# Kernel optimization log

Hardware: AMD Instinct MI355X
Metric: run time of the kernel (lower is better)

Reference implementation:

```python
import jax, jax.numpy as jnp
import numpy as np

KERNEL_LEN = 512
INPUT_LEN = 65536


def setup_inputs() -> dict:
    key = jax.random.key(0)
    k1, k2 = jax.random.split(key)
    x = jax.random.normal(k1, (INPUT_LEN,), dtype=jnp.float32)
    kernel = jax.random.normal(k2, (KERNEL_LEN,), dtype=jnp.float32)
    return {"input": x, "kernel": kernel}


def _dtw_row(prev, d_row):
    # prev: accumulated_cost of previous row, shape [K]
    # ac[j] = min(prev[j-1], prev[j], ac[j-1]) + d[j]
    # Let c[j] = min(prev[j-1], prev[j]) + d[j]  (prev[-1] treated as +inf,
    # which reproduces ac[i,0] = prev[0] + d[0]).
    # Then ac[j] = min(c[j], ac[j-1] + d[j])
    #            = S[j] + cummin_k<=j (c[k] - S[k]),  S = inclusive cumsum of d.
    inf = jnp.full((1,), jnp.inf, dtype=d_row.dtype)
    prev_shift = jnp.concatenate([inf, prev[:-1]])
    c = jnp.minimum(prev_shift, prev) + d_row
    S = jnp.cumsum(d_row)
    ac = S + jax.lax.cummin(c - S)
    return ac, ac[-1]


def reference(input, kernel):
    # pairwise squared distances: [input_len, kernel_len]
    d = (kernel[None, :] - input[:, None]) ** 2
    # row 0: cumulative sum along kernel axis
    prev0 = jnp.cumsum(d[0])
    # rows 1..N-1 via scan with wavefront-free min-plus row update
    _, lasts = jax.lax.scan(_dtw_row, prev0, d[1:])
    # return accumulated_cost[:, kernel_len - 1]
    return jnp.concatenate([prev0[-1:], lasts])
```

## Files before the change

### kernel.cpp

```cpp
#include <hip/hip_runtime.h>


#define K_LEN 512
#define N_LEN 65536
#define PAD_L 512
#define PAD_R 1024
#define XPAD_TOTAL (PAD_L + N_LEN + PAD_R)
#define BIGX 1e20f
#define NCHUNK 1032
#define RING 256

#define DPPF(old, src, ctrl)                                                     \
    __int_as_float(__builtin_amdgcn_update_dpp(                                  \
        __float_as_int(old), __float_as_int(src), (ctrl), 0xF, 0xF, false))

__global__ void dtw_pad_kernel(const float* __restrict__ x, float* __restrict__ xpad) {
    int i = blockIdx.x * blockDim.x + threadIdx.x;
    if (i < XPAD_TOTAL) {
        int j = i - PAD_L;
        xpad[i] = (j >= 0 && j < N_LEN) ? x[j] : BIGX;
    }
}

template <bool LAST>
__device__ __forceinline__ void dtw_chunk(int c, float& Xa, const float* __restrict__ xlw,
                                          const float* __restrict__ ldsIn,
                                          float* __restrict__ ldsOut,
                                          float k0, float k1,
                                          float& A0, float& A1, float& E0, float& E1,
                                          float& xA, float& xB, int lane,
                                          float* __restrict__ out) {
    const int t0 = c * 64;
    const int rb = (c & 3) * 64;

    const float Xb = xlw[t0 + 64 + lane];

    float B = ldsIn[(rb + lane + RING - 1) & (RING - 1)];

    float X = Xa;
    float C = 0.0f;

#pragma unroll
    for (int r = 0; r < 64; ++r) {
        const float xnew = DPPF(X, xB, 0x138);
        const float esh0 = DPPF(B, E1, 0x138);
        X = DPPF(X, X, 0x130);
        B = DPPF(B, B, 0x130);
        float d0 = k0 - xnew; d0 *= d0;
        float d1 = k1 - xA;   d1 *= d1;
        const float na0 = fminf(A0, esh0) + d0;
        const float na1 = fminf(A1, E0) + d1;
        const float ne0 = fminf(na0, A0);
        const float ne1 = fminf(na1, A1);
        C = DPPF(LAST ? na1 : ne1, C, 0x130);
        A0 = na0; A1 = na1; E0 = ne0; E1 = ne1;
        xB = xA; xA = xnew;
    }

    Xa = Xb;
    if (!LAST) {
        ldsOut[rb + lane] = C;
    } else {
        const int oi = t0 + lane - (K_LEN - 1);
        if (oi >= 0 && oi < N_LEN) out[oi] = C;
    }
}

__global__ __launch_bounds__(256, 1) void dtw_main(const float* __restrict__ xpad,
                                                   const float* __restrict__ kern,
                                                   float* __restrict__ out) {
    __shared__ float lds[5 * RING];
    const float INFV = __builtin_inff();
    const int tid  = threadIdx.x;
    const int w    = __builtin_amdgcn_readfirstlane(tid) >> 6;
    const int lane = tid & 63;

    for (int i = tid; i < 5 * RING; i += 256)
        lds[i] = (i == 4 * RING + RING - 1) ? 0.0f : INFV;
    __syncthreads();

    const int j0 = w * 128 + 2 * lane;
    const float k0 = kern[j0];
    const float k1 = kern[j0 + 1];

    const float* xl  = xpad + PAD_L - j0;
    const float* xlw = xpad + PAD_L - w * 128;
    float xA = xl[-1];
    float xB = xl[-2];
    float Xa = xlw[lane];

    float* ldsOut      = lds + w * RING;
    const float* ldsIn = (w == 0) ? (lds + 4 * RING) : (lds + (w - 1) * RING);

    float A0 = INFV, A1 = INFV, E0 = INFV, E1 = INFV;

    for (int S = 0; S < NCHUNK + 3; ++S) {
        const int c = S - w;
        if (c >= 0 && c < NCHUNK) {
            if (w == 3)
                dtw_chunk<true>(c, Xa, xlw, ldsIn, ldsOut, k0, k1, A0, A1, E0, E1, xA, xB, lane, out);
            else
                dtw_chunk<false>(c, Xa, xlw, ldsIn, ldsOut, k0, k1, A0, A1, E0, E1, xA, xB, lane, out);
        }
        if (S == 0 && tid == 0) lds[4 * RING + RING - 1] = INFV;
        __syncthreads();
    }
}

extern "C" void kernel_launch(void* const* d_in, const int* in_sizes, int n_in,
                              void* d_out, int out_size, void* d_ws, size_t ws_size,
                              hipStream_t stream) {
    const float* x = (const float*)d_in[0];
    const float* k = (const float*)d_in[1];
    float* xpad = (float*)d_ws;
    float* out  = (float*)d_out;
    dtw_pad_kernel<<<(XPAD_TOTAL + 255) / 256, 256, 0, stream>>>(x, xpad);
    dtw_main<<<1, 256, 0, stream>>>(xpad, k, out);
}
```

Measured before the change: 2.277 ms.

## Spread DTW across eight waves with one column per lane and register x buffers

Doubles the wavefront pipeline from four to eight waves, so each lane now owns one kernel column instead of two. The per-row input values are no longer passed between lanes with DPP shifts. Each lane instead preloads 64 diagonal-indexed x values from global memory into double-buffered register arrays, and the distance is folded into an FMA. This shortens the per-row serial work per lane and puts two waves on each SIMD to interleave. The costs are 64 global loads per lane per chunk, heavy register use, and a longer pipeline fill and drain.

New measurement: 2.986 ms. 1.31x slower.

```diff
diff --git a/kernel.cpp b/kernel.cpp
--- a/kernel.cpp
+++ b/kernel.cpp
@@ -9,6 +9,8 @@
 #define BIGX 1e20f
 #define NCHUNK 1032
 #define RING 256
+#define NWAVE 8
+#define INIT_RING 7
 
 #define DPPF(old, src, ctrl)                                                     \
     __int_as_float(__builtin_amdgcn_update_dpp(                                  \
@@ -23,41 +25,33 @@
 }
 
 template <bool LAST>
-__device__ __forceinline__ void dtw_chunk(int c, float& Xa, const float* __restrict__ xlw,
+__device__ __forceinline__ void dtw_chunk(int c, const float* __restrict__ xl,
+                                          float (&xc)[64], float (&xn)[64],
                                           const float* __restrict__ ldsIn,
                                           float* __restrict__ ldsOut,
-                                          float k0, float k1,
-                                          float& A0, float& A1, float& E0, float& E1,
-                                          float& xA, float& xB, int lane,
-                                          float* __restrict__ out) {
+                                          float kk, float& A, float& E,
+                                          int lane, float* __restrict__ out) {
     const int t0 = c * 64;
     const int rb = (c & 3) * 64;
 
-    const float Xb = xlw[t0 + 64 + lane];
+#pragma unroll
+    for (int q = 0; q < 64; ++q) xn[q] = xl[t0 + 64 + q];
 
     float B = ldsIn[(rb + lane + RING - 1) & (RING - 1)];
 
-    float X = Xa;
     float C = 0.0f;
 
 #pragma unroll
     for (int r = 0; r < 64; ++r) {
-        const float xnew = DPPF(X, xB, 0x138);
-        const float esh0 = DPPF(B, E1, 0x138);
-        X = DPPF(X, X, 0x130);
+        const float esh = DPPF(B, E, 0x138);
         B = DPPF(B, B, 0x130);
-        float d0 = k0 - xnew; d0 *= d0;
-        float d1 = k1 - xA;   d1 *= d1;
-        const float na0 = fminf(A0, esh0) + d0;
-        const float na1 = fminf(A1, E0) + d1;
-        const float ne0 = fminf(na0, A0);
-        const float ne1 = fminf(na1, A1);
-        C = DPPF(LAST ? na1 : ne1, C, 0x130);
-        A0 = na0; A1 = na1; E0 = ne0; E1 = ne1;
-        xB = xA; xA = xnew;
+        const float t = kk - xc[r];
+        const float na = __builtin_fmaf(t, t, fminf(A, esh));
+        const float ne = fminf(na, A);
+        C = DPPF(LAST ? na : ne, C, 0x130);
+        A = na; E = ne;
     }
 
-    Xa = Xb;
     if (!LAST) {
         ldsOut[rb + lane] = C;
     } else {
@@ -66,43 +60,45 @@
     }
 }
 
-__global__ __launch_bounds__(256, 1) void dtw_main(const float* __restrict__ xpad,
+__global__ __launch_bounds__(512, 1) void dtw_main(const float* __restrict__ xpad,
                                                    const float* __restrict__ kern,
                                                    float* __restrict__ out) {
-    __shared__ float lds[5 * RING];
+    __shared__ float lds[NWAVE * RING];
     const float INFV = __builtin_inff();
     const int tid  = threadIdx.x;
     const int w    = __builtin_amdgcn_readfirstlane(tid) >> 6;
     const int lane = tid & 63;
 
-    for (int i = tid; i < 5 * RING; i += 256)
-        lds[i] = (i == 4 * RING + RING - 1) ? 0.0f : INFV;
+    for (int i = tid; i < NWAVE * RING; i += 512)
+        lds[i] = (i == INIT_RING * RING + RING - 1) ? 0.0f : INFV;
     __syncthreads();
 
-    const int j0 = w * 128 + 2 * lane;
-    const float k0 = kern[j0];
-    const float k1 = kern[j0 + 1];
+    const int j0 = w * 64 + lane;
+    const float kk = kern[j0];
 
-    const float* xl  = xpad + PAD_L - j0;
-    const float* xlw = xpad + PAD_L - w * 128;
-    float xA = xl[-1];
-    float xB = xl[-2];
-    float Xa = xlw[lane];
+    const float* xl = xpad + PAD_L - j0;
 
     float* ldsOut      = lds + w * RING;
-    const float* ldsIn = (w == 0) ? (lds + 4 * RING) : (lds + (w - 1) * RING);
+    const float* ldsIn = (w == 0) ? (lds + INIT_RING * RING) : (lds + (w - 1) * RING);
 
-    float A0 = INFV, A1 = INFV, E0 = INFV, E1 = INFV;
+    float A = INFV, E = INFV;
 
-    for (int S = 0; S < NCHUNK + 3; ++S) {
+    float xwA[64], xwB[64];
+#pragma unroll
+    for (int q = 0; q < 64; ++q) xwA[q] = xl[q];
+
+    for (int S = 0; S < NCHUNK + NWAVE - 1; ++S) {
         const int c = S - w;
         if (c >= 0 && c < NCHUNK) {
-            if (w == 3)
-                dtw_chunk<true>(c, Xa, xlw, ldsIn, ldsOut, k0, k1, A0, A1, E0, E1, xA, xB, lane, out);
-            else
-                dtw_chunk<false>(c, Xa, xlw, ldsIn, ldsOut, k0, k1, A0, A1, E0, E1, xA, xB, lane, out);
+            if (c & 1) {
+                if (w == NWAVE - 1) dtw_chunk<true >(c, xl, xwB, xwA, ldsIn, ldsOut, kk, A, E, lane, out);
+                else                dtw_chunk<false>(c, xl, xwB, xwA, ldsIn, ldsOut, kk, A, E, lane, out);
+            } else {
+                if (w == NWAVE - 1) dtw_chunk<true >(c, xl, xwA, xwB, ldsIn, ldsOut, kk, A, E, lane, out);
+                else                dtw_chunk<false>(c, xl, xwA, xwB, ldsIn, ldsOut, kk, A, E, lane, out);
+            }
         }
-        if (S == 0 && tid == 0) lds[4 * RING + RING - 1] = INFV;
+        if (S == 0 && tid == 0) lds[INIT_RING * RING + RING - 1] = INFV;
         __syncthreads();
     }
 }
@@ -115,5 +111,5 @@
     float* xpad = (float*)d_ws;
     float* out  = (float*)d_out;
     dtw_pad_kernel<<<(XPAD_TOTAL + 255) / 256, 256, 0, stream>>>(x, xpad);
-    dtw_main<<<1, 256, 0, stream>>>(xpad, k, out);
+    dtw_main<<<1, 512, 0, stream>>>(xpad, k, out);
 }
```
